# Kernel optimization log

Hardware: AMD Instinct MI355X
Metric: run time of the kernel (lower is better)

The kernel has to match this reference:

```python
import jax, jax.numpy as jnp
import numpy as np

BLOCK_SIZE = 128
FP8_MAX = 448.0
IN_FEATURES = 4096
OUT_FEATURES = 4096


def _fp8_round(x):
    # Simulate float8_e4m3fn storage; fall back to clamp-only if dtype unsupported.
    try:
        return x.astype(jnp.float8_e4m3fn).astype(jnp.float32)
    except Exception:
        return x


def setup_inputs() -> dict:
    key = jax.random.key(0)
    kx, kw = jax.random.split(key)
    x = jax.random.normal(kx, (2, 4096, IN_FEATURES), dtype=jnp.float32)
    # Kaiming-uniform-ish init, then block-quantize exactly as fp8_block_quantize does.
    bound = 1.0 / np.sqrt(IN_FEATURES)
    w = jax.random.uniform(kw, (OUT_FEATURES, IN_FEATURES), minval=-bound, maxval=bound, dtype=jnp.float32)
    w_blocks = w.reshape(-1, BLOCK_SIZE)  # (n_blocks, 128); 4096*4096 divisible by 128
    block_abs_max = jnp.maximum(jnp.max(jnp.abs(w_blocks), axis=-1), 1e-12)
    fp8_scales = block_abs_max / FP8_MAX  # (n_blocks,)
    w_scaled = jnp.clip(w_blocks / fp8_scales[:, None], -FP8_MAX, FP8_MAX)
    weight_q = _fp8_round(w_scaled).reshape(OUT_FEATURES, IN_FEATURES)
    bias = jnp.zeros((OUT_FEATURES,), dtype=jnp.float32)
    return {"x": x, "weight_q": weight_q, "fp8_scales": fp8_scales, "bias": bias}


def reference(x, weight_q, fp8_scales, bias):
    # Block-wise dequantize: flatten weight, scale each 128-element block.
    w_blocks = weight_q.reshape(-1, BLOCK_SIZE)            # (n_blocks, 128)
    w = (w_blocks * fp8_scales[:, None]).reshape(OUT_FEATURES, IN_FEATURES)
    # F.linear: y = x @ w.T + b
    return jnp.einsum('bsk,nk->bsn', x, w) + bias
```

## Files before the change

### kernel.cpp

```cpp
#include <hip/hip_runtime.h>


#define M_DIM 8192
#define N_DIM 4096
#define K_DIM 4096

typedef short s16x8 __attribute__((ext_vector_type(8)));
typedef float f32x4 __attribute__((ext_vector_type(4)));

__device__ __forceinline__ unsigned short f32_to_bf16(float f) {
    unsigned int u = __float_as_uint(f);
    unsigned int r = (u + 0x7fffu + ((u >> 16) & 1u)) >> 16;
    return (unsigned short)r;
}

__device__ __forceinline__ ushort4 pack4(float4 a) {
    ushort4 r;
    r.x = f32_to_bf16(a.x); r.y = f32_to_bf16(a.y);
    r.z = f32_to_bf16(a.z); r.w = f32_to_bf16(a.w);
    return r;
}

__global__ __launch_bounds__(256) void cvt_fused_kernel(
    const float4* __restrict__ x, const float4* __restrict__ wq,
    const float* __restrict__ scales,
    ushort4* __restrict__ xo, ushort4* __restrict__ wo) {
    const int b = blockIdx.x;
    const int t = threadIdx.x;
    if (b < 16384) {
        const int base = b * 512 + t;
#pragma unroll
        for (int j = 0; j < 2; ++j) {
            const int idx = base + j * 256;
            xo[idx] = pack4(x[idx]);
        }
    } else {
        const int base = (b - 16384) * 512 + t;
#pragma unroll
        for (int j = 0; j < 2; ++j) {
            const int idx = base + j * 256;
            const float s = scales[idx >> 5];
            float4 a = wq[idx];
            a.x *= s; a.y *= s; a.z *= s; a.w *= s;
            wo[idx] = pack4(a);
        }
    }
}

__device__ __forceinline__ void async_copy16(const unsigned short* g, unsigned short* l) {
    __builtin_amdgcn_global_load_lds(
        (const __attribute__((address_space(1))) unsigned int*)g,
        (__attribute__((address_space(3))) unsigned int*)l,
        16, 0, 0);
}

__global__ __launch_bounds__(256) void gemm_bt_kernel(
    const unsigned short* __restrict__ A,
    const unsigned short* __restrict__ B,
    const float* __restrict__ bias,
    float* __restrict__ C)
{
    __shared__ unsigned short lds_a[128 * 32];
    __shared__ unsigned short lds_b[128 * 32];

    const int t = threadIdx.x;
    const int w = t >> 6;
    const int l = t & 63;
    const int m0 = blockIdx.y * 128;
    const int n0 = blockIdx.x * 128;
    const int wm = (w & 1) * 64;
    const int wn = (w >> 1) * 64;

    const int srow = t >> 2;
    const int scol = (t & 3) * 8;
    const unsigned short* gA = A + (long)(m0 + srow) * K_DIM + scol;
    const unsigned short* gB = B + (long)(n0 + srow) * K_DIM + scol;
    unsigned short* lA = lds_a + t * 8;
    unsigned short* lB = lds_b + t * 8;

    const int fr = l & 15;
    const int fc = (l >> 4) * 8;

    f32x4 acc[4][4] = {};

    for (int kt = 0; kt < K_DIM / 32; ++kt) {
        const unsigned short* ga = gA + kt * 32;
        const unsigned short* gb = gB + kt * 32;
        async_copy16(ga,              lA);
        async_copy16(ga + 64 * K_DIM, lA + 2048);
        async_copy16(gb,              lB);
        async_copy16(gb + 64 * K_DIM, lB + 2048);
        __syncthreads();

        s16x8 af[4], bf[4];
#pragma unroll
        for (int i = 0; i < 4; ++i)
            af[i] = *(const s16x8*)(lds_a + (wm + i * 16 + fr) * 32 + fc);
#pragma unroll
        for (int j = 0; j < 4; ++j)
            bf[j] = *(const s16x8*)(lds_b + (wn + j * 16 + fr) * 32 + fc);

#pragma unroll
        for (int i = 0; i < 4; ++i)
#pragma unroll
            for (int j = 0; j < 4; ++j)
                acc[i][j] = __builtin_amdgcn_mfma_f32_16x16x32_bf16(
                    af[i], bf[j], acc[i][j], 0, 0, 0);
        __syncthreads();
    }

    const int q = l >> 4;
#pragma unroll
    for (int j = 0; j < 4; ++j) {
        const int col = n0 + wn + j * 16 + (l & 15);
        const float bv = bias[col];
#pragma unroll
        for (int i = 0; i < 4; ++i) {
            const int row = m0 + wm + i * 16 + q * 4;
#pragma unroll
            for (int r = 0; r < 4; ++r) {
                C[(long)(row + r) * N_DIM + col] = acc[i][j][r] + bv;
            }
        }
    }
}

extern "C" void kernel_launch(void* const* d_in, const int* in_sizes, int n_in,
                              void* d_out, int out_size, void* d_ws, size_t ws_size,
                              hipStream_t stream) {
    const float* x      = (const float*)d_in[0];
    const float* wq     = (const float*)d_in[1];
    const float* scales = (const float*)d_in[2];
    const float* bias   = (const float*)d_in[3];
    float* out = (float*)d_out;

    unsigned short* x_bf = (unsigned short*)d_ws;
    unsigned short* w_bf = x_bf + (size_t)M_DIM * K_DIM;

    cvt_fused_kernel<<<24576, 256, 0, stream>>>(
        (const float4*)x, (const float4*)wq, scales,
        (ushort4*)x_bf, (ushort4*)w_bf);

    dim3 grid(N_DIM / 128, M_DIM / 128);
    gemm_bt_kernel<<<grid, 256, 0, stream>>>(x_bf, w_bf, bias, out);
}
```

Baseline: 564.9 us.

## Rewrite GEMM as 256x256 double-buffered pipelined kernel with swizzled LDS

```diff
diff --git a/kernel.cpp b/kernel.cpp
--- a/kernel.cpp
+++ b/kernel.cpp
@@ -4,6 +4,7 @@
 #define M_DIM 8192
 #define N_DIM 4096
 #define K_DIM 4096
+#define K_TILES (K_DIM / 64)
 
 typedef short s16x8 __attribute__((ext_vector_type(8)));
 typedef float f32x4 __attribute__((ext_vector_type(4)));
@@ -47,79 +48,126 @@
     }
 }
 
-__device__ __forceinline__ void async_copy16(const unsigned short* g, unsigned short* l) {
+__device__ __forceinline__ void async_copy16(const void* g, void* l) {
     __builtin_amdgcn_global_load_lds(
         (const __attribute__((address_space(1))) unsigned int*)g,
         (__attribute__((address_space(3))) unsigned int*)l,
         16, 0, 0);
 }
 
-__global__ __launch_bounds__(256) void gemm_bt_kernel(
+
+#define STAGE_A_HALF(h, ktt, bufb) do {                                        \
+    const unsigned short* g_ = gA0 + (ktt) * 64 + (h) * (64 * K_DIM);          \
+    async_copy16(g_,               ldsA + (bufb) + (h) * 8192 + aOff);         \
+    async_copy16(g_ + 128 * K_DIM, ldsA + (bufb) + (h) * 8192 + 16384 + aOff); \
+  } while (0)
+
+#define STAGE_B_HALF(h, ktt, bufb) do {                                        \
+    const unsigned short* g_ = gB0 + (ktt) * 64 + (h) * (32 * K_DIM);          \
+    async_copy16(g_,               ldsB + (bufb) + (h) * 4096 + bOff);         \
+    async_copy16(g_ + 128 * K_DIM, ldsB + (bufb) + (h) * 4096 + 16384 + bOff); \
+  } while (0)
+
+#define PHASE(qm, qn, bufb, STAGE_STMT, WAITN) do {                            \
+    STAGE_STMT;                                                                \
+    asm volatile("s_waitcnt vmcnt(" #WAITN ")" ::: "memory");                  \
+    __builtin_amdgcn_s_barrier();                                              \
+    asm volatile("" ::: "memory");                                             \
+    __builtin_amdgcn_sched_barrier(0);                                         \
+    s16x8 af[4][2], bf[2][2];                                                  \
+    _Pragma("unroll")                                                          \
+    for (int i = 0; i < 4; ++i) {                                              \
+      af[i][0] = *(const s16x8*)(ldsA + (bufb) + aRowB + ((qm)*64 + i*16)*128 + kk0); \
+      af[i][1] = *(const s16x8*)(ldsA + (bufb) + aRowB + ((qm)*64 + i*16)*128 + kk1); \
+    }                                                                          \
+    _Pragma("unroll")                                                          \
+    for (int j = 0; j < 2; ++j) {                                              \
+      bf[j][0] = *(const s16x8*)(ldsB + (bufb) + bRowB + ((qn)*32 + j*16)*128 + kk0); \
+      bf[j][1] = *(const s16x8*)(ldsB + (bufb) + bRowB + ((qn)*32 + j*16)*128 + kk1); \
+    }                                                                          \
+    __builtin_amdgcn_s_setprio(1);                                             \
+    _Pragma("unroll")                                                          \
+    for (int i = 0; i < 4; ++i)                                                \
+      _Pragma("unroll")                                                        \
+      for (int j = 0; j < 2; ++j) {                                            \
+        acc[(qm)*4+i][(qn)*2+j] = __builtin_amdgcn_mfma_f32_16x16x32_bf16(     \
+            af[i][0], bf[j][0], acc[(qm)*4+i][(qn)*2+j], 0, 0, 0);             \
+        acc[(qm)*4+i][(qn)*2+j] = __builtin_amdgcn_mfma_f32_16x16x32_bf16(     \
+            af[i][1], bf[j][1], acc[(qm)*4+i][(qn)*2+j], 0, 0, 0);             \
+      }                                                                        \
+    __builtin_amdgcn_s_setprio(0);                                             \
+  } while (0)
+
+__global__ __launch_bounds__(512, 2) void gemm_bt_kernel(
     const unsigned short* __restrict__ A,
     const unsigned short* __restrict__ B,
     const float* __restrict__ bias,
     float* __restrict__ C)
 {
-    __shared__ unsigned short lds_a[128 * 32];
-    __shared__ unsigned short lds_b[128 * 32];
+    __shared__ __align__(16) char lds[131072];
+    char* ldsA = lds;
+    char* ldsB = lds + 32768;
 
     const int t = threadIdx.x;
+    const int l = t & 63;
     const int w = t >> 6;
-    const int l = t & 63;
-    const int m0 = blockIdx.y * 128;
-    const int n0 = blockIdx.x * 128;
-    const int wm = (w & 1) * 64;
-    const int wn = (w >> 1) * 64;
+    const int wr = w >> 2;
+    const int wc = w & 3;
 
-    const int srow = t >> 2;
-    const int scol = (t & 3) * 8;
-    const unsigned short* gA = A + (long)(m0 + srow) * K_DIM + scol;
-    const unsigned short* gB = B + (long)(n0 + srow) * K_DIM + scol;
-    unsigned short* lA = lds_a + t * 8;
-    unsigned short* lB = lds_b + t * 8;
+    int id = blockIdx.x;
+    id = (id & 7) * 64 + (id >> 3);
+    const int m0 = (id >> 4) * 256;
+    const int n0 = (id & 15) * 256;
 
-    const int fr = l & 15;
-    const int fc = (l >> 4) * 8;
+    const int trow = t >> 3;
+    const int tcol = ((t & 7) * 8) ^ ((trow & 7) * 8);
+    const unsigned short* gA0 = A + (long)(m0 + trow) * K_DIM + tcol;
+    const int brow = ((t >> 8) * 64) + ((t & 255) >> 3);
+    const unsigned short* gB0 = B + (long)(n0 + brow) * K_DIM + tcol;
+    const int aOff = t * 16;
+    const int bOff = ((t >> 8) * 8192) + ((t & 255) * 16);
 
-    f32x4 acc[4][4] = {};
+    const int aRowB = (wr * 128 + (l & 15)) * 128;
+    const int bRowB = (wc * 64  + (l & 15)) * 128;
+    const int kx  = (l >> 4) * 16;
+    const int sw  = (l & 7) * 16;
+    const int kk0 = kx ^ sw;
+    const int kk1 = (64 + kx) ^ sw;
 
-    for (int kt = 0; kt < K_DIM / 32; ++kt) {
-        const unsigned short* ga = gA + kt * 32;
-        const unsigned short* gb = gB + kt * 32;
-        async_copy16(ga,              lA);
-        async_copy16(ga + 64 * K_DIM, lA + 2048);
-        async_copy16(gb,              lB);
-        async_copy16(gb + 64 * K_DIM, lB + 2048);
-        __syncthreads();
+    f32x4 acc[8][4] = {};
 
-        s16x8 af[4], bf[4];
-#pragma unroll
-        for (int i = 0; i < 4; ++i)
-            af[i] = *(const s16x8*)(lds_a + (wm + i * 16 + fr) * 32 + fc);
-#pragma unroll
-        for (int j = 0; j < 4; ++j)
-            bf[j] = *(const s16x8*)(lds_b + (wn + j * 16 + fr) * 32 + fc);
+    STAGE_A_HALF(0, 0, 0);
+    STAGE_B_HALF(0, 0, 0);
+    STAGE_B_HALF(1, 0, 0);
+    STAGE_A_HALF(1, 0, 0);
 
-#pragma unroll
-        for (int i = 0; i < 4; ++i)
-#pragma unroll
-            for (int j = 0; j < 4; ++j)
-                acc[i][j] = __builtin_amdgcn_mfma_f32_16x16x32_bf16(
-                    af[i], bf[j], acc[i][j], 0, 0, 0);
-        __syncthreads();
+    for (int kt = 0; kt < K_TILES - 1; ++kt) {
+        const int cb = (kt & 1) * 65536;
+        const int nb = 65536 - cb;
+        PHASE(0, 0, cb, STAGE_A_HALF(0, kt + 1, nb), 6);
+        PHASE(0, 1, cb, STAGE_B_HALF(0, kt + 1, nb), 6);
+        PHASE(1, 0, cb, STAGE_B_HALF(1, kt + 1, nb), 6);
+        PHASE(1, 1, cb, STAGE_A_HALF(1, kt + 1, nb), 6);
+    }
+    {
+        const int cb = ((K_TILES - 1) & 1) * 65536;
+        PHASE(0, 0, cb, (void)0, 4);
+        PHASE(0, 1, cb, (void)0, 2);
+        PHASE(1, 0, cb, (void)0, 0);
+        PHASE(1, 1, cb, (void)0, 0);
     }
 
-    const int q = l >> 4;
+    const int q4 = (l >> 4) * 4;
 #pragma unroll
-    for (int j = 0; j < 4; ++j) {
-        const int col = n0 + wn + j * 16 + (l & 15);
+    for (int nf = 0; nf < 4; ++nf) {
+        const int col = n0 + wc * 64 + nf * 16 + (l & 15);
         const float bv = bias[col];
 #pragma unroll
-        for (int i = 0; i < 4; ++i) {
-            const int row = m0 + wm + i * 16 + q * 4;
+        for (int mf = 0; mf < 8; ++mf) {
+            const long row = m0 + wr * 128 + mf * 16 + q4;
 #pragma unroll
             for (int r = 0; r < 4; ++r) {
-                C[(long)(row + r) * N_DIM + col] = acc[i][j][r] + bv;
+                C[(row + r) * N_DIM + col] = acc[mf][nf][r] + bv;
             }
         }
     }
@@ -141,6 +189,5 @@
         (const float4*)x, (const float4*)wq, scales,
         (ushort4*)x_bf, (ushort4*)w_bf);
 
-    dim3 grid(N_DIM / 128, M_DIM / 128);
-    gemm_bt_kernel<<<grid, 256, 0, stream>>>(x_bf, w_bf, bias, out);
+    gemm_bt_kernel<<<dim3(512), dim3(512), 0, stream>>>(x_bf, w_bf, bias, out);
 }
```

Measured after the change: 510.1 us. 1.11x faster.
